# Kernel tuning notes

Hardware: AMD Instinct MI355X
Metric: run time of the kernel (lower is better)

The kernel has to match this reference:

```python
import jax, jax.numpy as jnp
import numpy as np

N = 50000       # nodes
E = 800000      # edges (avg degree 16)
C_IN = 128
C_OUT = 128
RATIO = 0.5
K = int(np.ceil(RATIO * N))  # static top-k size (single graph)
EPS = 1e-5      # BatchNorm eps


def setup_inputs() -> dict:
    key = jax.random.key(0)
    ks = jax.random.split(key, 12)
    x = jax.random.normal(ks[0], (N, C_IN), jnp.float32)
    edge_index = jax.random.randint(ks[1], (2, E), 0, N, dtype=jnp.int32)
    batch = jnp.zeros((N,), jnp.int32)
    s_in = 1.0 / np.sqrt(C_IN)
    s_out = 1.0 / np.sqrt(C_OUT)
    return {
        "x": x,
        "edge_index": edge_index,
        "batch": batch,
        "lin_w": jax.random.uniform(ks[2], (C_IN, C_OUT), jnp.float32, -s_in, s_in),
        "lin_b": jax.random.uniform(ks[3], (C_OUT,), jnp.float32, -s_in, s_in),
        "bn1_g": jnp.ones((C_OUT,), jnp.float32),
        "bn1_b": jnp.zeros((C_OUT,), jnp.float32),
        "gcn_w": jax.random.uniform(ks[4], (C_OUT, C_OUT), jnp.float32, -s_out, s_out),
        "gcn_b": jnp.zeros((C_OUT,), jnp.float32),
        "bn2_g": jnp.ones((C_OUT,), jnp.float32),
        "bn2_b": jnp.zeros((C_OUT,), jnp.float32),
        "pool_w": jax.random.uniform(ks[5], (C_OUT,), jnp.float32, -s_out, s_out),
    }


def _batchnorm(h, g, b):
    # training-mode BatchNorm1d: biased variance over the node axis
    mu = jnp.mean(h, axis=0)
    var = jnp.mean(jnp.square(h - mu), axis=0)
    return (h - mu) * jax.lax.rsqrt(var + EPS) * g + b


def reference(x, edge_index, batch, lin_w, lin_b, bn1_g, bn1_b,
              gcn_w, gcn_b, bn2_g, bn2_b, pool_w):
    # ---- MLP: Linear + BN + ReLU ----
    h = jax.nn.relu(_batchnorm(x @ lin_w + lin_b, bn1_g, bn1_b))

    # ---- GCNConv with self-loops + symmetric normalization ----
    loops = jnp.arange(N, dtype=edge_index.dtype)
    row = jnp.concatenate([edge_index[0], loops])  # source
    col = jnp.concatenate([edge_index[1], loops])  # target
    hw = h @ gcn_w                                    # [N, C_OUT]
    deg = jax.ops.segment_sum(jnp.ones_like(col, jnp.float32), col, num_segments=N)
    dinv = jnp.where(deg > 0, jax.lax.rsqrt(deg), 0.0)
    norm = dinv[row] * dinv[col]                      # [E+N]
    agg = jax.ops.segment_sum(hw[row] * norm[:, None], col, num_segments=N)
    out = agg + gcn_b

    # ---- BN + ReLU ----
    h2 = jax.nn.relu(_batchnorm(out, bn2_g, bn2_b))

    # ---- TopKPooling (single graph -> static k) ----
    score = jnp.tanh((h2 @ pool_w) / jnp.linalg.norm(pool_w))
    top_score, perm = jax.lax.top_k(score, K)
    x_pool = h2[perm] * top_score[:, None]            # [K, C_OUT]
    batch_new = batch[perm]

    # filter_adj with fixed shape: dropped edges marked -1
    mask = jnp.zeros((N,), bool).at[perm].set(True)
    new_idx = jnp.full((N,), -1, edge_index.dtype).at[perm].set(
        jnp.arange(K, dtype=edge_index.dtype))
    src, dst = edge_index[0], edge_index[1]
    keep = mask[src] & mask[dst]
    ei_new = jnp.where(keep[None, :],
                       jnp.stack([new_idx[src], new_idx[dst]]),
                       jnp.array(-1, edge_index.dtype))
    return x_pool, ei_new, batch_new
```

## Files before the change

### kernel.cpp

```cpp
#include <hip/hip_runtime.h>
#include <hip/hip_bf16.h>

#define NN 50000
#define EE 800000
#define KTOP 25000
#define EPSF 1e-5

__global__ __launch_bounds__(256, 2) void gemm_bn_stats(const float* __restrict__ A,
                                                        const float* __restrict__ W,
                                                        const float* __restrict__ bias,
                                                        float* __restrict__ Y,
                                                        double* __restrict__ part, int M) {
    __shared__ float Bs[128][128];
    __shared__ float As[32][132];
    int t = threadIdx.x;
    int bm = blockIdx.x * 128;

    const float4* W4 = (const float4*)W;
    float4* Bs4 = (float4*)Bs;
#pragma unroll
    for (int i = 0; i < 16; i++) Bs4[t + i * 256] = W4[t + i * 256];

    float acc[8][8];
#pragma unroll
    for (int i = 0; i < 8; i++)
#pragma unroll
        for (int j = 0; j < 8; j++) acc[i][j] = 0.f;

    int ty = t >> 4;
    int tx = t & 15;

    for (int kc = 0; kc < 4; kc++) {
        __syncthreads();
#pragma unroll
        for (int i = 0; i < 4; i++) {
            int f4 = t + i * 256;
            int r = f4 >> 3, k4 = f4 & 7;
            int row = bm + r;
            float4 v = make_float4(0.f, 0.f, 0.f, 0.f);
            if (row < M) v = *(const float4*)&A[(size_t)row * 128 + kc * 32 + k4 * 4];
            As[k4 * 4 + 0][r] = v.x;
            As[k4 * 4 + 1][r] = v.y;
            As[k4 * 4 + 2][r] = v.z;
            As[k4 * 4 + 3][r] = v.w;
        }
        __syncthreads();
#pragma unroll
        for (int kk = 0; kk < 32; kk++) {
            float4 a0 = *(float4*)&As[kk][ty * 8];
            float4 a1 = *(float4*)&As[kk][ty * 8 + 4];
            float4 b0 = *(float4*)&Bs[kc * 32 + kk][tx * 4];
            float4 b1 = *(float4*)&Bs[kc * 32 + kk][64 + tx * 4];
            float av[8] = {a0.x, a0.y, a0.z, a0.w, a1.x, a1.y, a1.z, a1.w};
            float bv[8] = {b0.x, b0.y, b0.z, b0.w, b1.x, b1.y, b1.z, b1.w};
#pragma unroll
            for (int i = 0; i < 8; i++)
#pragma unroll
                for (int j = 0; j < 8; j++) acc[i][j] += av[i] * bv[j];
        }
    }

    float4 bb0 = *(const float4*)&bias[tx * 4];
    float4 bb1 = *(const float4*)&bias[64 + tx * 4];
    float s[8], s2[8];
#pragma unroll
    for (int j = 0; j < 8; j++) { s[j] = 0.f; s2[j] = 0.f; }
#pragma unroll
    for (int i = 0; i < 8; i++) {
        int row = bm + ty * 8 + i;
        if (row < M) {
            float4 y0, y1;
            y0.x = acc[i][0] + bb0.x; y0.y = acc[i][1] + bb0.y;
            y0.z = acc[i][2] + bb0.z; y0.w = acc[i][3] + bb0.w;
            y1.x = acc[i][4] + bb1.x; y1.y = acc[i][5] + bb1.y;
            y1.z = acc[i][6] + bb1.z; y1.w = acc[i][7] + bb1.w;
            *(float4*)&Y[(size_t)row * 128 + tx * 4] = y0;
            *(float4*)&Y[(size_t)row * 128 + 64 + tx * 4] = y1;
            s[0] += y0.x; s2[0] += y0.x * y0.x;
            s[1] += y0.y; s2[1] += y0.y * y0.y;
            s[2] += y0.z; s2[2] += y0.z * y0.z;
            s[3] += y0.w; s2[3] += y0.w * y0.w;
            s[4] += y1.x; s2[4] += y1.x * y1.x;
            s[5] += y1.y; s2[5] += y1.y * y1.y;
            s[6] += y1.z; s2[6] += y1.z * y1.z;
            s[7] += y1.w; s2[7] += y1.w * y1.w;
        }
    }
    __syncthreads();
    float2* Sred = (float2*)As;
#pragma unroll
    for (int j = 0; j < 8; j++) {
        int col = (j < 4) ? (tx * 4 + j) : (64 + tx * 4 + j - 4);
        Sred[ty * 128 + col] = make_float2(s[j], s2[j]);
    }
    __syncthreads();
    if (t < 128) {
        double S = 0.0, S2 = 0.0;
#pragma unroll
        for (int r = 0; r < 16; r++) {
            float2 v = Sred[r * 128 + t];
            S += (double)v.x;
            S2 += (double)v.y;
        }
        part[((size_t)blockIdx.x * 128 + t) * 2 + 0] = S;
        part[((size_t)blockIdx.x * 128 + t) * 2 + 1] = S2;
    }
}

__global__ __launch_bounds__(256, 2) void gemm_bn_apply(const float* __restrict__ Yin,
                                                        const float* __restrict__ W,
                                                        const float* __restrict__ sc,
                                                        const float* __restrict__ sh,
                                                        const float* __restrict__ dinv,
                                                        float* __restrict__ HWs, int M) {
    __shared__ float Bs[128][128];
    __shared__ float As[32][132];
    int t = threadIdx.x;
    int bm = blockIdx.x * 128;

    const float4* W4 = (const float4*)W;
    float4* Bs4 = (float4*)Bs;
#pragma unroll
    for (int i = 0; i < 16; i++) Bs4[t + i * 256] = W4[t + i * 256];

    float acc[8][8];
#pragma unroll
    for (int i = 0; i < 8; i++)
#pragma unroll
        for (int j = 0; j < 8; j++) acc[i][j] = 0.f;

    int ty = t >> 4;
    int tx = t & 15;

    for (int kc = 0; kc < 4; kc++) {
        __syncthreads();
#pragma unroll
        for (int i = 0; i < 4; i++) {
            int f4 = t + i * 256;
            int r = f4 >> 3, k4 = f4 & 7;
            int row = bm + r;
            int col = kc * 32 + k4 * 4;
            float4 v = make_float4(0.f, 0.f, 0.f, 0.f);
            if (row < M) {
                float4 y = *(const float4*)&Yin[(size_t)row * 128 + col];
                float4 scv = *(const float4*)&sc[col];
                float4 shv = *(const float4*)&sh[col];
                v.x = fmaxf(y.x * scv.x + shv.x, 0.f);
                v.y = fmaxf(y.y * scv.y + shv.y, 0.f);
                v.z = fmaxf(y.z * scv.z + shv.z, 0.f);
                v.w = fmaxf(y.w * scv.w + shv.w, 0.f);
            }
            As[k4 * 4 + 0][r] = v.x;
            As[k4 * 4 + 1][r] = v.y;
            As[k4 * 4 + 2][r] = v.z;
            As[k4 * 4 + 3][r] = v.w;
        }
        __syncthreads();
#pragma unroll
        for (int kk = 0; kk < 32; kk++) {
            float4 a0 = *(float4*)&As[kk][ty * 8];
            float4 a1 = *(float4*)&As[kk][ty * 8 + 4];
            float4 b0 = *(float4*)&Bs[kc * 32 + kk][tx * 4];
            float4 b1 = *(float4*)&Bs[kc * 32 + kk][64 + tx * 4];
            float av[8] = {a0.x, a0.y, a0.z, a0.w, a1.x, a1.y, a1.z, a1.w};
            float bv[8] = {b0.x, b0.y, b0.z, b0.w, b1.x, b1.y, b1.z, b1.w};
#pragma unroll
            for (int i = 0; i < 8; i++)
#pragma unroll
                for (int j = 0; j < 8; j++) acc[i][j] += av[i] * bv[j];
        }
    }
#pragma unroll
    for (int i = 0; i < 8; i++) {
        int row = bm + ty * 8 + i;
        if (row < M) {
            float di = dinv[row];
            float4 o0, o1;
            o0.x = acc[i][0] * di; o0.y = acc[i][1] * di;
            o0.z = acc[i][2] * di; o0.w = acc[i][3] * di;
            o1.x = acc[i][4] * di; o1.y = acc[i][5] * di;
            o1.z = acc[i][6] * di; o1.w = acc[i][7] * di;
            *(float4*)&HWs[(size_t)row * 128 + tx * 4] = o0;
            *(float4*)&HWs[(size_t)row * 128 + 64 + tx * 4] = o1;
        }
    }
}

#define BN2_ROWS 64
#define BN2_NB ((NN + BN2_ROWS - 1) / BN2_ROWS)

__global__ __launch_bounds__(128) void bn_stats(const float* __restrict__ Y,
                                                double* __restrict__ part, int M) {
    int c = threadIdx.x;
    int b = blockIdx.x;
    int r0 = b * BN2_ROWS;
    int r1 = min(M, r0 + BN2_ROWS);
    double s = 0.0, s2 = 0.0;
    int r = r0;
    for (; r + 4 <= r1; r += 4) {
        float v0 = Y[(size_t)r * 128 + c];
        float v1 = Y[(size_t)(r + 1) * 128 + c];
        float v2 = Y[(size_t)(r + 2) * 128 + c];
        float v3 = Y[(size_t)(r + 3) * 128 + c];
        s += (double)v0 + (double)v1 + (double)v2 + (double)v3;
        s2 += (double)v0 * v0 + (double)v1 * v1 + (double)v2 * v2 + (double)v3 * v3;
    }
    for (; r < r1; r++) {
        float v = Y[(size_t)r * 128 + c];
        s += (double)v;
        s2 += (double)v * v;
    }
    part[((size_t)b * 128 + c) * 2 + 0] = s;
    part[((size_t)b * 128 + c) * 2 + 1] = s2;
}

__global__ __launch_bounds__(256) void bn_finalize(const double* __restrict__ part, int nb,
                                                   const float* __restrict__ g,
                                                   const float* __restrict__ beta,
                                                   float* __restrict__ scale,
                                                   float* __restrict__ shift, int M) {
    int c = blockIdx.x;
    int t = threadIdx.x;
    double s = 0.0, s2 = 0.0;
    for (int b = t; b < nb; b += 256) {
        s += part[((size_t)b * 128 + c) * 2 + 0];
        s2 += part[((size_t)b * 128 + c) * 2 + 1];
    }
    __shared__ double sd[256], sd2[256];
    sd[t] = s;
    sd2[t] = s2;
    __syncthreads();
#pragma unroll
    for (int o = 128; o > 0; o >>= 1) {
        if (t < o) {
            sd[t] += sd[t + o];
            sd2[t] += sd2[t + o];
        }
        __syncthreads();
    }
    if (t == 0) {
        double S = sd[0], S2 = sd2[0];
        double mu = S / (double)M;
        double var = S2 / (double)M - mu * mu;
        double inv = 1.0 / sqrt(var + (double)EPSF);
        scale[c] = (float)((double)g[c] * inv);
        shift[c] = (float)((double)beta[c] - mu * (double)g[c] * inv);
    }
}

__global__ __launch_bounds__(256) void count_deg(const int* __restrict__ col,
                                                 int* __restrict__ cnt, int E) {
    int e = blockIdx.x * 256 + threadIdx.x;
    if (e < E) atomicAdd(&cnt[col[e]], 1);
}

__global__ __launch_bounds__(256) void fill_csr(const int* __restrict__ row,
                                                const int* __restrict__ col,
                                                const int* __restrict__ off,
                                                int* __restrict__ cur,
                                                int* __restrict__ csr, int E) {
    int e = blockIdx.x * 256 + threadIdx.x;
    if (e < E) {
        int c = col[e];
        int p = atomicAdd(&cur[c], 1);
        csr[off[c] + p] = row[e];
    }
}

__device__ __forceinline__ int waveInclScan(int v, int lane) {
#pragma unroll
    for (int o = 1; o < 64; o <<= 1) {
        int u = __shfl_up(v, o, 64);
        if (lane >= o) v += u;
    }
    return v;
}

__global__ __launch_bounds__(1024) void scan_phase1(const int* __restrict__ in,
                                                    int* __restrict__ out,
                                                    int* __restrict__ bsum,
                                                    float* __restrict__ dinv, int n) {
    int t = threadIdx.x;
    int g = blockIdx.x * 1024 + t;
    int lane = t & 63, wid = t >> 6;
    int v = (g < n) ? in[g] : 0;
    if (dinv && g < n) dinv[g] = (float)(1.0 / sqrt((double)(v + 1)));
    int incl = waveInclScan(v, lane);
    __shared__ int ws[16];
    if (lane == 63) ws[wid] = incl;
    __syncthreads();
    if (t < 16) {
        int x = ws[t];
#pragma unroll
        for (int o = 1; o < 16; o <<= 1) {
            int u = __shfl_up(x, o, 64);
            if (t >= o) x += u;
        }
        ws[t] = x;
    }
    __syncthreads();
    int pre = (wid > 0) ? ws[wid - 1] : 0;
    if (g < n) out[g] = pre + incl - v;
    if (t == 1023) bsum[blockIdx.x] = ws[15];
}

__global__ __launch_bounds__(1024) void scan_phase2(int* __restrict__ bsum, int B,
                                                    int* __restrict__ out, int n) {
    int t = threadIdx.x;
    int lane = t & 63, wid = t >> 6;
    int v = (t < B) ? bsum[t] : 0;
    int incl = waveInclScan(v, lane);
    __shared__ int ws[16];
    if (lane == 63) ws[wid] = incl;
    __syncthreads();
    if (t < 16) {
        int x = ws[t];
#pragma unroll
        for (int o = 1; o < 16; o <<= 1) {
            int u = __shfl_up(x, o, 64);
            if (t >= o) x += u;
        }
        ws[t] = x;
    }
    __syncthreads();
    int pre = (wid > 0) ? ws[wid - 1] : 0;
    int glob_incl = pre + incl;
    if (t < B) bsum[t] = glob_incl - v;
    if (t == B - 1) out[n] = glob_incl;
}

__global__ __launch_bounds__(1024) void scan_phase3(int* __restrict__ out,
                                                    const int* __restrict__ bsum, int n) {
    int g = blockIdx.x * 1024 + threadIdx.x;
    if (g < n) out[g] += bsum[blockIdx.x];
}

__global__ __launch_bounds__(256) void gcn_agg(const float* __restrict__ HWs,
                                               const int* __restrict__ off,
                                               const int* __restrict__ csr,
                                               const float* __restrict__ dinv,
                                               const float* __restrict__ gcn_b,
                                               float* __restrict__ OUT, int M) {
    int lane = threadIdx.x & 63;
    int i = blockIdx.x * 4 + (threadIdx.x >> 6);
    if (i >= M) return;
    const float2* H2 = (const float2*)HWs;
    int o0 = off[i], o1 = off[i + 1];
    float2 hv = H2[(size_t)i * 64 + lane];
    double ax = (double)hv.x, ay = (double)hv.y;
    int e = o0;
    for (; e + 8 <= o1; e += 8) {
        int s0 = csr[e], s1 = csr[e + 1], s2 = csr[e + 2], s3 = csr[e + 3];
        int s4 = csr[e + 4], s5 = csr[e + 5], s6 = csr[e + 6], s7 = csr[e + 7];
        float2 v0 = H2[(size_t)s0 * 64 + lane];
        float2 v1 = H2[(size_t)s1 * 64 + lane];
        float2 v2 = H2[(size_t)s2 * 64 + lane];
        float2 v3 = H2[(size_t)s3 * 64 + lane];
        float2 v4 = H2[(size_t)s4 * 64 + lane];
        float2 v5 = H2[(size_t)s5 * 64 + lane];
        float2 v6 = H2[(size_t)s6 * 64 + lane];
        float2 v7 = H2[(size_t)s7 * 64 + lane];
        ax += ((double)v0.x + (double)v1.x) + ((double)v2.x + (double)v3.x) +
              ((double)v4.x + (double)v5.x) + ((double)v6.x + (double)v7.x);
        ay += ((double)v0.y + (double)v1.y) + ((double)v2.y + (double)v3.y) +
              ((double)v4.y + (double)v5.y) + ((double)v6.y + (double)v7.y);
    }
    for (; e < o1; e++) {
        float2 v = H2[(size_t)csr[e] * 64 + lane];
        ax += (double)v.x;
        ay += (double)v.y;
    }
    double di = (double)dinv[i];
    float2 ob = ((const float2*)gcn_b)[lane];
    float2 o;
    o.x = (float)(ax * di) + ob.x;
    o.y = (float)(ay * di) + ob.y;
    ((float2*)OUT)[(size_t)i * 64 + lane] = o;
}

__global__ __launch_bounds__(256) void score_key(const float* __restrict__ Y2,
                                                 const float* __restrict__ sc,
                                                 const float* __restrict__ sh,
                                                 const float* __restrict__ w,
                                                 float* __restrict__ score,
                                                 unsigned* __restrict__ key,
                                                 int* __restrict__ bcnt, int M) {
    int lane = threadIdx.x & 63;
    int wid = threadIdx.x >> 6;
    int gw = blockIdx.x * 4 + wid;
    int nw = gridDim.x * 4;

    float w0 = w[lane], w1 = w[lane + 64];
    float sc0 = sc[lane], sh0 = sh[lane];
    float sc1 = sc[lane + 64], sh1 = sh[lane + 64];

    float nv = w0 * w0 + w1 * w1;
#pragma unroll
    for (int o = 32; o >= 1; o >>= 1) nv += __shfl_xor(nv, o, 64);
    float nrm = sqrtf(nv);

    for (int r = gw; r < M; r += nw) {
        float a = Y2[(size_t)r * 128 + lane];
        float b = Y2[(size_t)r * 128 + lane + 64];
        a = fmaxf(a * sc0 + sh0, 0.f);
        b = fmaxf(b * sc1 + sh1, 0.f);
        float v = a * w0 + b * w1;
#pragma unroll
        for (int o = 32; o >= 1; o >>= 1) v += __shfl_xor(v, o, 64);
        if (lane == 0) {
            score[r] = tanhf(v / nrm);
            unsigned u = __float_as_uint(v);
            unsigned k = (u & 0x80000000u) ? ~u : (u | 0x80000000u);
            key[r] = k;
            atomicAdd(&bcnt[k >> 16], 1);
        }
    }
}

__global__ __launch_bounds__(256) void bucket_fill(const unsigned* __restrict__ key,
                                                   const int* __restrict__ boff,
                                                   int* __restrict__ bcur,
                                                   int* __restrict__ bmem, int M) {
    int i = blockIdx.x * 256 + threadIdx.x;
    if (i < M) {
        int b = key[i] >> 16;
        int p = atomicAdd(&bcur[b], 1);
        bmem[boff[b] + p] = i;
    }
}

__global__ __launch_bounds__(256) void rank_kernel(const unsigned* __restrict__ key,
                                                   const int* __restrict__ boff,
                                                   const int* __restrict__ bmem,
                                                   int* __restrict__ rank,
                                                   int* __restrict__ nidx, int M) {
    int i = blockIdx.x * 256 + threadIdx.x;
    if (i >= M) return;
    unsigned ki = key[i];
    int b = ki >> 16;
    int r = M - boff[b + 1];
    int p0 = boff[b], p1 = boff[b + 1];
    for (int p = p0; p < p1; p++) {
        int j = bmem[p];
        unsigned kj = key[j];
        if (kj > ki || (kj == ki && j < i)) r++;
    }
    rank[i] = r;
    nidx[i] = (r < KTOP) ? r : -1;
}

__global__ __launch_bounds__(128) void write_pool(const float* __restrict__ Y2,
                                                  const float* __restrict__ sc,
                                                  const float* __restrict__ sh,
                                                  const float* __restrict__ score,
                                                  const int* __restrict__ rank,
                                                  float* __restrict__ out0,
                                                  float* __restrict__ out2, int M) {
    int sub = threadIdx.x >> 5;
    int c4 = threadIdx.x & 31;
    int i = blockIdx.x * 4 + sub;
    if (i >= M) return;
    int r = rank[i];
    if (r < KTOP) {
        float s = score[i];
        float4 y = *(const float4*)&Y2[(size_t)i * 128 + c4 * 4];
        float4 scv = *(const float4*)&sc[c4 * 4];
        float4 shv = *(const float4*)&sh[c4 * 4];
        float4 o;
        o.x = fmaxf(y.x * scv.x + shv.x, 0.f) * s;
        o.y = fmaxf(y.y * scv.y + shv.y, 0.f) * s;
        o.z = fmaxf(y.z * scv.z + shv.z, 0.f) * s;
        o.w = fmaxf(y.w * scv.w + shv.w, 0.f) * s;
        *(float4*)&out0[(size_t)r * 128 + c4 * 4] = o;
        if (c4 == 0) out2[r] = 0.0f;
    }
}

__global__ __launch_bounds__(256) void write_edges(const int* __restrict__ row,
                                                   const int* __restrict__ col,
                                                   const int* __restrict__ nidx,
                                                   float* __restrict__ out1, int E) {
    int e = blockIdx.x * 256 + threadIdx.x;
    if (e < E) {
        int a = nidx[row[e]];
        int b = nidx[col[e]];
        bool keep = (a >= 0) && (b >= 0);
        out1[e] = keep ? (float)a : -1.0f;
        out1[E + e] = keep ? (float)b : -1.0f;
    }
}

extern "C" void kernel_launch(void* const* d_in, const int* in_sizes, int n_in,
                              void* d_out, int out_size, void* d_ws, size_t ws_size,
                              hipStream_t stream) {
    const float* x = (const float*)d_in[0];
    const int* ei = (const int*)d_in[1];
    const float* lin_w = (const float*)d_in[3];
    const float* lin_b = (const float*)d_in[4];
    const float* bn1_g = (const float*)d_in[5];
    const float* bn1_b = (const float*)d_in[6];
    const float* gcn_w = (const float*)d_in[7];
    const float* gcn_b = (const float*)d_in[8];
    const float* bn2_g = (const float*)d_in[9];
    const float* bn2_b = (const float*)d_in[10];
    const float* pool_w = (const float*)d_in[11];

    const int* e_row = ei;
    const int* e_col = ei + EE;

    char* ws = (char*)d_ws;
    size_t off_b = 0;
    auto alloc = [&](size_t bytes) -> void* {
        void* p = ws + off_b;
        off_b = (off_b + bytes + 255) & ~(size_t)255;
        return p;
    };
    float* y = (float*)alloc((size_t)NN * 128 * 4);
    float* hws = (float*)alloc((size_t)NN * 128 * 4);
    int* cnt = (int*)alloc(NN * 4);
    int* cur = (int*)alloc(NN * 4);
    int* offs = (int*)alloc((NN + 1) * 4);
    float* dinv = (float*)alloc(NN * 4);
    int* csr = (int*)alloc((size_t)EE * 4);
    float* score = (float*)alloc(NN * 4);
    unsigned* key = (unsigned*)alloc(NN * 4);
    int* rank = (int*)alloc(NN * 4);
    int* nidx = (int*)alloc(NN * 4);
    int* bcnt = (int*)alloc(65536 * 4);
    int* boff = (int*)alloc((65536 + 1) * 4);
    int* bcur = (int*)alloc(65536 * 4);
    int* bmem = (int*)alloc(NN * 4);
    double* part = (double*)alloc((size_t)BN2_NB * 128 * 2 * 8);
    float* scale1 = (float*)alloc(128 * 4);
    float* shift1 = (float*)alloc(128 * 4);
    float* scale2 = (float*)alloc(128 * 4);
    float* shift2 = (float*)alloc(128 * 4);
    int* bsum = (int*)alloc(128 * 4);

    float* out0 = (float*)d_out;
    float* out1 = out0 + (size_t)KTOP * 128;
    float* out2 = out1 + (size_t)2 * EE;

    int gemm_grid = (NN + 127) / 128;

    hipMemsetAsync(cnt, 0, NN * 4, stream);
    hipMemsetAsync(cur, 0, NN * 4, stream);
    hipMemsetAsync(bcnt, 0, 65536 * 4, stream);
    hipMemsetAsync(bcur, 0, 65536 * 4, stream);
    count_deg<<<(EE + 255) / 256, 256, 0, stream>>>(e_col, cnt, EE);
    {
        int B = (NN + 1023) / 1024;
        scan_phase1<<<B, 1024, 0, stream>>>(cnt, offs, bsum, dinv, NN);
        scan_phase2<<<1, 1024, 0, stream>>>(bsum, B, offs, NN);
        scan_phase3<<<B, 1024, 0, stream>>>(offs, bsum, NN);
    }
    fill_csr<<<(EE + 255) / 256, 256, 0, stream>>>(e_row, e_col, offs, cur, csr, EE);

    gemm_bn_stats<<<gemm_grid, 256, 0, stream>>>(x, lin_w, lin_b, y, part, NN);
    bn_finalize<<<128, 256, 0, stream>>>(part, gemm_grid, bn1_g, bn1_b, scale1, shift1, NN);

    gemm_bn_apply<<<gemm_grid, 256, 0, stream>>>(y, gcn_w, scale1, shift1, dinv, hws, NN);
    gcn_agg<<<(NN + 3) / 4, 256, 0, stream>>>(hws, offs, csr, dinv, gcn_b, y, NN);

    bn_stats<<<BN2_NB, 128, 0, stream>>>(y, part, NN);
    bn_finalize<<<128, 256, 0, stream>>>(part, BN2_NB, bn2_g, bn2_b, scale2, shift2, NN);

    score_key<<<512, 256, 0, stream>>>(y, scale2, shift2, pool_w, score, key, bcnt, NN);
    {
        int B = 65536 / 1024;
        scan_phase1<<<B, 1024, 0, stream>>>(bcnt, boff, bsum, nullptr, 65536);
        scan_phase2<<<1, 1024, 0, stream>>>(bsum, B, boff, 65536);
        scan_phase3<<<B, 1024, 0, stream>>>(boff, bsum, 65536);
    }
    bucket_fill<<<(NN + 255) / 256, 256, 0, stream>>>(key, boff, bcur, bmem, NN);
    rank_kernel<<<(NN + 255) / 256, 256, 0, stream>>>(key, boff, bmem, rank, nidx, NN);

    write_pool<<<(NN + 3) / 4, 128, 0, stream>>>(y, scale2, shift2, score, rank, out0, out2, NN);
    write_edges<<<(EE + 255) / 256, 256, 0, stream>>>(e_row, e_col, nidx, out1, EE);
}
```

Before: 363.0 us.

## Fuse BN2 statistics into GCN aggregation and widen gather to float4 half-waves

```diff
diff --git a/kernel.cpp b/kernel.cpp
--- a/kernel.cpp
+++ b/kernel.cpp
@@ -186,34 +186,6 @@
     }
 }
 
-#define BN2_ROWS 64
-#define BN2_NB ((NN + BN2_ROWS - 1) / BN2_ROWS)
-
-__global__ __launch_bounds__(128) void bn_stats(const float* __restrict__ Y,
-                                                double* __restrict__ part, int M) {
-    int c = threadIdx.x;
-    int b = blockIdx.x;
-    int r0 = b * BN2_ROWS;
-    int r1 = min(M, r0 + BN2_ROWS);
-    double s = 0.0, s2 = 0.0;
-    int r = r0;
-    for (; r + 4 <= r1; r += 4) {
-        float v0 = Y[(size_t)r * 128 + c];
-        float v1 = Y[(size_t)(r + 1) * 128 + c];
-        float v2 = Y[(size_t)(r + 2) * 128 + c];
-        float v3 = Y[(size_t)(r + 3) * 128 + c];
-        s += (double)v0 + (double)v1 + (double)v2 + (double)v3;
-        s2 += (double)v0 * v0 + (double)v1 * v1 + (double)v2 * v2 + (double)v3 * v3;
-    }
-    for (; r < r1; r++) {
-        float v = Y[(size_t)r * 128 + c];
-        s += (double)v;
-        s2 += (double)v * v;
-    }
-    part[((size_t)b * 128 + c) * 2 + 0] = s;
-    part[((size_t)b * 128 + c) * 2 + 1] = s2;
-}
-
 __global__ __launch_bounds__(256) void bn_finalize(const double* __restrict__ part, int nb,
                                                    const float* __restrict__ g,
                                                    const float* __restrict__ beta,
@@ -225,6 +197,41 @@
     for (int b = t; b < nb; b += 256) {
         s += part[((size_t)b * 128 + c) * 2 + 0];
         s2 += part[((size_t)b * 128 + c) * 2 + 1];
+    }
+    __shared__ double sd[256], sd2[256];
+    sd[t] = s;
+    sd2[t] = s2;
+    __syncthreads();
+#pragma unroll
+    for (int o = 128; o > 0; o >>= 1) {
+        if (t < o) {
+            sd[t] += sd[t + o];
+            sd2[t] += sd2[t + o];
+        }
+        __syncthreads();
+    }
+    if (t == 0) {
+        double S = sd[0], S2 = sd2[0];
+        double mu = S / (double)M;
+        double var = S2 / (double)M - mu * mu;
+        double inv = 1.0 / sqrt(var + (double)EPSF);
+        scale[c] = (float)((double)g[c] * inv);
+        shift[c] = (float)((double)beta[c] - mu * (double)g[c] * inv);
+    }
+}
+
+__global__ __launch_bounds__(256) void bn_finalize2(const float2* __restrict__ part, int nb,
+                                                    const float* __restrict__ g,
+                                                    const float* __restrict__ beta,
+                                                    float* __restrict__ scale,
+                                                    float* __restrict__ shift, int M) {
+    int c = blockIdx.x;
+    int t = threadIdx.x;
+    double s = 0.0, s2 = 0.0;
+    for (int b = t; b < nb; b += 256) {
+        float2 v = part[(size_t)b * 128 + c];
+        s += (double)v.x;
+        s2 += (double)v.y;
     }
     __shared__ double sd[256], sd2[256];
     sd[t] = s;
@@ -335,47 +342,85 @@
     if (g < n) out[g] += bsum[blockIdx.x];
 }
 
-__global__ __launch_bounds__(256) void gcn_agg(const float* __restrict__ HWs,
+__global__ __launch_bounds__(512) void gcn_agg(const float* __restrict__ HWs,
                                                const int* __restrict__ off,
                                                const int* __restrict__ csr,
                                                const float* __restrict__ dinv,
                                                const float* __restrict__ gcn_b,
-                                               float* __restrict__ OUT, int M) {
-    int lane = threadIdx.x & 63;
-    int i = blockIdx.x * 4 + (threadIdx.x >> 6);
-    if (i >= M) return;
-    const float2* H2 = (const float2*)HWs;
-    int o0 = off[i], o1 = off[i + 1];
-    float2 hv = H2[(size_t)i * 64 + lane];
-    double ax = (double)hv.x, ay = (double)hv.y;
-    int e = o0;
-    for (; e + 8 <= o1; e += 8) {
-        int s0 = csr[e], s1 = csr[e + 1], s2 = csr[e + 2], s3 = csr[e + 3];
-        int s4 = csr[e + 4], s5 = csr[e + 5], s6 = csr[e + 6], s7 = csr[e + 7];
-        float2 v0 = H2[(size_t)s0 * 64 + lane];
-        float2 v1 = H2[(size_t)s1 * 64 + lane];
-        float2 v2 = H2[(size_t)s2 * 64 + lane];
-        float2 v3 = H2[(size_t)s3 * 64 + lane];
-        float2 v4 = H2[(size_t)s4 * 64 + lane];
-        float2 v5 = H2[(size_t)s5 * 64 + lane];
-        float2 v6 = H2[(size_t)s6 * 64 + lane];
-        float2 v7 = H2[(size_t)s7 * 64 + lane];
-        ax += ((double)v0.x + (double)v1.x) + ((double)v2.x + (double)v3.x) +
-              ((double)v4.x + (double)v5.x) + ((double)v6.x + (double)v7.x);
-        ay += ((double)v0.y + (double)v1.y) + ((double)v2.y + (double)v3.y) +
-              ((double)v4.y + (double)v5.y) + ((double)v6.y + (double)v7.y);
-    }
-    for (; e < o1; e++) {
-        float2 v = H2[(size_t)csr[e] * 64 + lane];
-        ax += (double)v.x;
-        ay += (double)v.y;
-    }
-    double di = (double)dinv[i];
-    float2 ob = ((const float2*)gcn_b)[lane];
-    float2 o;
-    o.x = (float)(ax * di) + ob.x;
-    o.y = (float)(ay * di) + ob.y;
-    ((float2*)OUT)[(size_t)i * 64 + lane] = o;
+                                               float* __restrict__ OUT,
+                                               float2* __restrict__ part32, int M) {
+    int t = threadIdx.x;
+    int w = t >> 6;
+    int lane = t & 63;
+    int half = lane >> 5;
+    int l32 = lane & 31;
+    int i = blockIdx.x * 8 + w;
+
+    const float4* H4 = (const float4*)HWs;
+    double a0 = 0.0, a1 = 0.0, a2 = 0.0, a3 = 0.0;
+
+    if (i < M) {
+        int o0 = off[i], o1 = off[i + 1];
+        if (half == 0) {
+            float4 sv = H4[(size_t)i * 32 + l32];
+            a0 = sv.x; a1 = sv.y; a2 = sv.z; a3 = sv.w;
+        }
+        int e = o0;
+        for (; e + 4 <= o1; e += 4) {
+            int sA = csr[e + half];
+            int sB = csr[e + 2 + half];
+            float4 vA = H4[(size_t)sA * 32 + l32];
+            float4 vB = H4[(size_t)sB * 32 + l32];
+            a0 += (double)vA.x + (double)vB.x;
+            a1 += (double)vA.y + (double)vB.y;
+            a2 += (double)vA.z + (double)vB.z;
+            a3 += (double)vA.w + (double)vB.w;
+        }
+        if (e + 2 <= o1) {
+            int sA = csr[e + half];
+            float4 vA = H4[(size_t)sA * 32 + l32];
+            a0 += (double)vA.x; a1 += (double)vA.y;
+            a2 += (double)vA.z; a3 += (double)vA.w;
+            e += 2;
+        }
+        if (e < o1 && half == 0) {
+            int sA = csr[e];
+            float4 vA = H4[(size_t)sA * 32 + l32];
+            a0 += (double)vA.x; a1 += (double)vA.y;
+            a2 += (double)vA.z; a3 += (double)vA.w;
+        }
+    }
+    a0 += __shfl_down(a0, 32, 64);
+    a1 += __shfl_down(a1, 32, 64);
+    a2 += __shfl_down(a2, 32, 64);
+    a3 += __shfl_down(a3, 32, 64);
+
+    __shared__ float2 sred[8][128];
+    if (i < M && half == 0) {
+        double di = (double)dinv[i];
+        float4 gb = ((const float4*)gcn_b)[l32];
+        float4 y;
+        y.x = (float)(a0 * di) + gb.x;
+        y.y = (float)(a1 * di) + gb.y;
+        y.z = (float)(a2 * di) + gb.z;
+        y.w = (float)(a3 * di) + gb.w;
+        ((float4*)OUT)[(size_t)i * 32 + l32] = y;
+        sred[w][l32 * 4 + 0] = make_float2(y.x, y.x * y.x);
+        sred[w][l32 * 4 + 1] = make_float2(y.y, y.y * y.y);
+        sred[w][l32 * 4 + 2] = make_float2(y.z, y.z * y.z);
+        sred[w][l32 * 4 + 3] = make_float2(y.w, y.w * y.w);
+    }
+    __syncthreads();
+    if (t < 128) {
+        float S = 0.f, S2 = 0.f;
+#pragma unroll
+        for (int ww = 0; ww < 8; ww++) {
+            float2 v = sred[ww][t];
+            S += v.x;
+            S2 += v.y;
+        }
+        part32[(size_t)blockIdx.x * 128 + t] = make_float2(S, S2);
+    }
 }
 
 __global__ __launch_bounds__(256) void score_key(const float* __restrict__ Y2,
@@ -527,10 +572,10 @@
     int* rank = (int*)alloc(NN * 4);
     int* nidx = (int*)alloc(NN * 4);
     int* bcnt = (int*)alloc(65536 * 4);
+    int* bcur = (int*)alloc(65536 * 4);
     int* boff = (int*)alloc((65536 + 1) * 4);
-    int* bcur = (int*)alloc(65536 * 4);
     int* bmem = (int*)alloc(NN * 4);
-    double* part = (double*)alloc((size_t)BN2_NB * 128 * 2 * 8);
+    double* part = (double*)alloc((size_t)400 * 128 * 2 * 8);
     float* scale1 = (float*)alloc(128 * 4);
     float* shift1 = (float*)alloc(128 * 4);
     float* scale2 = (float*)alloc(128 * 4);
@@ -541,12 +586,13 @@
     float* out1 = out0 + (size_t)KTOP * 128;
     float* out2 = out1 + (size_t)2 * EE;
 
+    float2* part32 = (float2*)out0;
+    int gcn_grid = (NN + 7) / 8;
+
     int gemm_grid = (NN + 127) / 128;
 
-    hipMemsetAsync(cnt, 0, NN * 4, stream);
-    hipMemsetAsync(cur, 0, NN * 4, stream);
-    hipMemsetAsync(bcnt, 0, 65536 * 4, stream);
-    hipMemsetAsync(bcur, 0, 65536 * 4, stream);
+    hipMemsetAsync(cnt, 0, (size_t)((char*)cur - (char*)cnt) + NN * 4, stream);
+    hipMemsetAsync(bcnt, 0, (size_t)((char*)bcur - (char*)bcnt) + 65536 * 4, stream);
     count_deg<<<(EE + 255) / 256, 256, 0, stream>>>(e_col, cnt, EE);
     {
         int B = (NN + 1023) / 1024;
@@ -560,10 +606,9 @@
     bn_finalize<<<128, 256, 0, stream>>>(part, gemm_grid, bn1_g, bn1_b, scale1, shift1, NN);
 
     gemm_bn_apply<<<gemm_grid, 256, 0, stream>>>(y, gcn_w, scale1, shift1, dinv, hws, NN);
-    gcn_agg<<<(NN + 3) / 4, 256, 0, stream>>>(hws, offs, csr, dinv, gcn_b, y, NN);
-
-    bn_stats<<<BN2_NB, 128, 0, stream>>>(y, part, NN);
-    bn_finalize<<<128, 256, 0, stream>>>(part, BN2_NB, bn2_g, bn2_b, scale2, shift2, NN);
+    gcn_agg<<<gcn_grid, 512, 0, stream>>>(hws, offs, csr, dinv, gcn_b, y, part32, NN);
+
+    bn_finalize2<<<128, 256, 0, stream>>>(part32, gcn_grid, bn2_g, bn2_b, scale2, shift2, NN);
 
     score_key<<<512, 256, 0, stream>>>(y, scale2, shift2, pool_w, score, key, bcnt, NN);
     {
```

New measurement: 366.4 us. No clear change (+0.9%).

## Stream weight tiles per K-chunk to cut LDS and merge memsets

Applied to the files above, without the earlier changes.

```diff
diff --git a/kernel.cpp b/kernel.cpp
--- a/kernel.cpp
+++ b/kernel.cpp
@@ -6,20 +6,17 @@
 #define KTOP 25000
 #define EPSF 1e-5
 
-__global__ __launch_bounds__(256, 2) void gemm_bn_stats(const float* __restrict__ A,
+__global__ __launch_bounds__(256, 4) void gemm_bn_stats(const float* __restrict__ A,
                                                         const float* __restrict__ W,
                                                         const float* __restrict__ bias,
                                                         float* __restrict__ Y,
                                                         double* __restrict__ part, int M) {
-    __shared__ float Bs[128][128];
+    __shared__ float Bsc[32][132];
     __shared__ float As[32][132];
     int t = threadIdx.x;
     int bm = blockIdx.x * 128;
 
     const float4* W4 = (const float4*)W;
-    float4* Bs4 = (float4*)Bs;
-#pragma unroll
-    for (int i = 0; i < 16; i++) Bs4[t + i * 256] = W4[t + i * 256];
 
     float acc[8][8];
 #pragma unroll
@@ -32,6 +29,13 @@
 
     for (int kc = 0; kc < 4; kc++) {
         __syncthreads();
+#pragma unroll
+        for (int i = 0; i < 4; i++) {
+            int f4 = t + i * 256;
+            int r = f4 >> 5, c = f4 & 31;
+            float4 wv = W4[(kc * 32 + r) * 32 + c];
+            *(float4*)&Bsc[r][c * 4] = wv;
+        }
 #pragma unroll
         for (int i = 0; i < 4; i++) {
             int f4 = t + i * 256;
@@ -49,8 +53,8 @@
         for (int kk = 0; kk < 32; kk++) {
             float4 a0 = *(float4*)&As[kk][ty * 8];
             float4 a1 = *(float4*)&As[kk][ty * 8 + 4];
-            float4 b0 = *(float4*)&Bs[kc * 32 + kk][tx * 4];
-            float4 b1 = *(float4*)&Bs[kc * 32 + kk][64 + tx * 4];
+            float4 b0 = *(float4*)&Bsc[kk][tx * 4];
+            float4 b1 = *(float4*)&Bsc[kk][64 + tx * 4];
             float av[8] = {a0.x, a0.y, a0.z, a0.w, a1.x, a1.y, a1.z, a1.w};
             float bv[8] = {b0.x, b0.y, b0.z, b0.w, b1.x, b1.y, b1.z, b1.w};
 #pragma unroll
@@ -107,21 +111,18 @@
     }
 }
 
-__global__ __launch_bounds__(256, 2) void gemm_bn_apply(const float* __restrict__ Yin,
+__global__ __launch_bounds__(256, 4) void gemm_bn_apply(const float* __restrict__ Yin,
                                                         const float* __restrict__ W,
                                                         const float* __restrict__ sc,
                                                         const float* __restrict__ sh,
                                                         const float* __restrict__ dinv,
                                                         float* __restrict__ HWs, int M) {
-    __shared__ float Bs[128][128];
+    __shared__ float Bsc[32][132];
     __shared__ float As[32][132];
     int t = threadIdx.x;
     int bm = blockIdx.x * 128;
 
     const float4* W4 = (const float4*)W;
-    float4* Bs4 = (float4*)Bs;
-#pragma unroll
-    for (int i = 0; i < 16; i++) Bs4[t + i * 256] = W4[t + i * 256];
 
     float acc[8][8];
 #pragma unroll
@@ -134,6 +135,13 @@
 
     for (int kc = 0; kc < 4; kc++) {
         __syncthreads();
+#pragma unroll
+        for (int i = 0; i < 4; i++) {
+            int f4 = t + i * 256;
+            int r = f4 >> 5, c = f4 & 31;
+            float4 wv = W4[(kc * 32 + r) * 32 + c];
+            *(float4*)&Bsc[r][c * 4] = wv;
+        }
 #pragma unroll
         for (int i = 0; i < 4; i++) {
             int f4 = t + i * 256;
@@ -160,8 +168,8 @@
         for (int kk = 0; kk < 32; kk++) {
             float4 a0 = *(float4*)&As[kk][ty * 8];
             float4 a1 = *(float4*)&As[kk][ty * 8 + 4];
-            float4 b0 = *(float4*)&Bs[kc * 32 + kk][tx * 4];
-            float4 b1 = *(float4*)&Bs[kc * 32 + kk][64 + tx * 4];
+            float4 b0 = *(float4*)&Bsc[kk][tx * 4];
+            float4 b1 = *(float4*)&Bsc[kk][64 + tx * 4];
             float av[8] = {a0.x, a0.y, a0.z, a0.w, a1.x, a1.y, a1.z, a1.w};
             float bv[8] = {b0.x, b0.y, b0.z, b0.w, b1.x, b1.y, b1.z, b1.w};
 #pragma unroll
@@ -527,8 +535,8 @@
     int* rank = (int*)alloc(NN * 4);
     int* nidx = (int*)alloc(NN * 4);
     int* bcnt = (int*)alloc(65536 * 4);
+    int* bcur = (int*)alloc(65536 * 4);
     int* boff = (int*)alloc((65536 + 1) * 4);
-    int* bcur = (int*)alloc(65536 * 4);
     int* bmem = (int*)alloc(NN * 4);
     double* part = (double*)alloc((size_t)BN2_NB * 128 * 2 * 8);
     float* scale1 = (float*)alloc(128 * 4);
@@ -543,10 +551,8 @@
 
     int gemm_grid = (NN + 127) / 128;
 
-    hipMemsetAsync(cnt, 0, NN * 4, stream);
-    hipMemsetAsync(cur, 0, NN * 4, stream);
-    hipMemsetAsync(bcnt, 0, 65536 * 4, stream);
-    hipMemsetAsync(bcur, 0, 65536 * 4, stream);
+    hipMemsetAsync(cnt, 0, (size_t)((char*)cur - (char*)cnt) + NN * 4, stream);
+    hipMemsetAsync(bcnt, 0, (size_t)((char*)bcur - (char*)bcnt) + 65536 * 4, stream);
     count_deg<<<(EE + 255) / 256, 256, 0, stream>>>(e_col, cnt, EE);
     {
         int B = (NN + 1023) / 1024;
```

Result: slower. 403.5 us (+11.2%).
